# Performance work log

Hardware: AMD Instinct MI355X
Metric: run time of the kernel (lower is better)

Reference implementation:

```python
import jax, jax.numpy as jnp
import numpy as np

NUM_HEADS = 8
NUM_GROUPS = 8
EPS = 1e-5


def group_norm(x, gamma, beta):
    # x: [B, C, H, W]; normalize over (C//G, H, W) per group
    B, C, H, W = x.shape
    xg = x.reshape(B, NUM_GROUPS, C // NUM_GROUPS, H, W)
    mean = jnp.mean(xg, axis=(2, 3, 4), keepdims=True)
    var = jnp.var(xg, axis=(2, 3, 4), keepdims=True)
    xg = (xg - mean) * jax.lax.rsqrt(var + EPS)
    x = xg.reshape(B, C, H, W)
    return x * gamma[None, :, None, None] + beta[None, :, None, None]


def setup_inputs() -> dict:
    key = jax.random.key(0)
    ks = jax.random.split(key, 10)
    B, C, H, W = 16, 512, 32, 32
    s = 0.02
    return {
        "x": jax.random.normal(ks[0], (B, C, H, W), jnp.float32),
        "wq": jax.random.normal(ks[1], (C, C), jnp.float32) * s,
        "bq": jnp.zeros((C,), jnp.float32),
        "wk": jax.random.normal(ks[2], (C, C), jnp.float32) * s,
        "bk": jnp.zeros((C,), jnp.float32),
        "wv": jax.random.normal(ks[3], (C, C), jnp.float32) * s,
        "bv": jnp.zeros((C,), jnp.float32),
        "wo": jax.random.normal(ks[4], (C, C), jnp.float32) * s,
        "bo": jnp.zeros((C,), jnp.float32),
        "gamma": jnp.ones((C,), jnp.float32),
        "beta": jnp.zeros((C,), jnp.float32),
    }


def reference(x, wq, bq, wk, bk, wv, bv, wo, bo, gamma, beta):
    B, C, H, W = x.shape
    Hh = NUM_HEADS
    Dh = C // Hh
    N = H * W
    scale = Dh ** (-0.5)

    residual = x
    xn = group_norm(x, gamma, beta).reshape(B, C, N)  # [B, C, N]

    # Conv1d kernel-size-1 == channel matmul: out[b,o,n] = sum_i w[o,i] x[b,i,n] + b[o]
    q = jnp.einsum('oi,bin->bon', wq, xn) + bq[None, :, None]
    k = jnp.einsum('oi,bin->bon', wk, xn) + bk[None, :, None]
    v = jnp.einsum('oi,bin->bon', wv, xn) + bv[None, :, None]

    q = q.reshape(B, Hh, Dh, N)
    k = k.reshape(B, Hh, Dh, N)
    v = v.reshape(B, Hh, Dh, N)

    attn = jnp.einsum('bhdn,bhdm->bhnm', q, k) * scale  # [B, H, N, N]
    attn = jax.nn.softmax(attn, axis=-1)
    out = jnp.einsum('bhnm,bhdm->bhdn', attn, v)  # [B, H, Dh, N]

    out = out.reshape(B, C, N)
    out = jnp.einsum('oi,bin->bon', wo, out) + bo[None, :, None]
    return out.reshape(B, C, H, W) + residual
```

## Files before the change

### kernel.cpp

```cpp
#include <hip/hip_runtime.h>
#include <hip/hip_bf16.h>

#define BB 16
#define CC 512
#define NN 1024
#define GG 8
#define HHH 8
#define DH 64

typedef __bf16 bf16x8 __attribute__((ext_vector_type(8)));
typedef float f32x4 __attribute__((ext_vector_type(4)));
typedef float f32x16 __attribute__((ext_vector_type(16)));
typedef unsigned int u32x4 __attribute__((ext_vector_type(4)));

#define QSCALE 0.18033688011116027f

__device__ __forceinline__ unsigned short bfb(float f) {
    __hip_bfloat16 h = __float2bfloat16(f);
    return __builtin_bit_cast(unsigned short, h);
}

__device__ __forceinline__ bf16x8 ldb8(const void* p) {
    return *reinterpret_cast<const bf16x8*>(p);
}

__device__ __forceinline__ unsigned int cvtpk(float lo, float hi) {
    unsigned int r;
    asm("v_cvt_pk_bf16_f32 %0, %1, %2" : "=v"(r) : "v"(lo), "v"(hi));
    return r;
}

typedef const __attribute__((address_space(1))) unsigned int* gas_ptr;
typedef __attribute__((address_space(3))) unsigned int* las_ptr;
__device__ __forceinline__ void gload_lds16(const void* g, void* l) {
    __builtin_amdgcn_global_load_lds((gas_ptr)g, (las_ptr)l, 16, 0, 0);
}

__global__ __launch_bounds__(256) void wconv_kernel(
    const float4* __restrict__ wq, const float4* __restrict__ wk,
    const float4* __restrict__ wv, const float4* __restrict__ wo,
    ushort4* __restrict__ oq, ushort4* __restrict__ ok2,
    ushort4* __restrict__ ov, ushort4* __restrict__ oo) {
    int i = blockIdx.x * 256 + threadIdx.x;
    float4 a;
    ushort4 r;
    a = wq[i]; r.x = bfb(a.x); r.y = bfb(a.y); r.z = bfb(a.z); r.w = bfb(a.w); oq[i] = r;
    a = wk[i]; r.x = bfb(a.x); r.y = bfb(a.y); r.z = bfb(a.z); r.w = bfb(a.w); ok2[i] = r;
    a = wv[i]; r.x = bfb(a.x); r.y = bfb(a.y); r.z = bfb(a.z); r.w = bfb(a.w); ov[i] = r;
    a = wo[i]; r.x = bfb(a.x); r.y = bfb(a.y); r.z = bfb(a.z); r.w = bfb(a.w); oo[i] = r;
}

__global__ __launch_bounds__(256) void gn_kernel(
    const float* __restrict__ x, const float* __restrict__ gamma,
    const float* __restrict__ beta, unsigned short* __restrict__ xnT) {
    int b = blockIdx.x >> 3, g = blockIdx.x & 7;
    const float* xg = x + ((size_t)b * CC + g * 64) * NN;
    int t = threadIdx.x;

    float s = 0.f, s2 = 0.f;
    for (int i = 0; i < 64; ++i) {
        float4 v = reinterpret_cast<const float4*>(xg)[t + i * 256];
        s += v.x + v.y + v.z + v.w;
        s2 += v.x * v.x + v.y * v.y + v.z * v.z + v.w * v.w;
    }
    #pragma unroll
    for (int m = 1; m < 64; m <<= 1) {
        s += __shfl_xor(s, m);
        s2 += __shfl_xor(s2, m);
    }
    __shared__ float red[2][4];
    int wid = t >> 6;
    if ((t & 63) == 0) { red[0][wid] = s; red[1][wid] = s2; }
    __syncthreads();
    s = red[0][0] + red[0][1] + red[0][2] + red[0][3];
    s2 = red[1][0] + red[1][1] + red[1][2] + red[1][3];
    float mean = s * (1.f / 65536.f);
    float var = s2 * (1.f / 65536.f) - mean * mean;
    float rstd = rsqrtf(var + 1e-5f);

    __shared__ unsigned short tile[64][68];
    for (int nt = 0; nt < 16; ++nt) {
        __syncthreads();
        #pragma unroll
        for (int p = 0; p < 4; ++p) {
            int cc = p * 16 + (t >> 4);
            int nn = (t & 15) * 4;
            float4 v = *reinterpret_cast<const float4*>(&xg[(size_t)cc * NN + nt * 64 + nn]);
            float ga = gamma[g * 64 + cc], be = beta[g * 64 + cc];
            float aa = rstd * ga;
            float c0 = be - mean * aa;
            ushort4 pk;
            pk.x = bfb(v.x * aa + c0);
            pk.y = bfb(v.y * aa + c0);
            pk.z = bfb(v.z * aa + c0);
            pk.w = bfb(v.w * aa + c0);
            *reinterpret_cast<ushort4*>(&tile[cc][nn]) = pk;
        }
        __syncthreads();
        #pragma unroll
        for (int p = 0; p < 16; ++p) {
            int nn = p * 4 + (t >> 6);
            int cc = t & 63;
            xnT[((size_t)b * NN + nt * 64 + nn) * CC + g * 64 + cc] = tile[cc][nn];
        }
    }
}

__global__ __launch_bounds__(256, 2) void qkv2_kernel(
    const unsigned short* __restrict__ wqb, const unsigned short* __restrict__ wkb,
    const unsigned short* __restrict__ wvb,
    const float* __restrict__ bq, const float* __restrict__ bk, const float* __restrict__ bv,
    const unsigned short* __restrict__ xnT,
    unsigned short* __restrict__ qt, unsigned short* __restrict__ kt,
    unsigned short* __restrict__ vv) {
    int wg = blockIdx.x;
    int xcd = wg & 7, local = wg >> 3;
    int mloc = local / 12;
    int rem = local - mloc * 12;
    int n_tile = rem / 3;
    int p = rem - n_tile * 3;
    int m_tile = xcd * 16 + mloc;

    const unsigned short* w = (p == 0) ? wqb : (p == 1) ? wkb : wvb;
    const float* bias = (p == 0) ? bq : (p == 1) ? bk : bv;
    int row0 = m_tile * 128;
    int o0t = n_tile * 128;

    __shared__ __align__(16) char As[2][16384];
    __shared__ __align__(16) char Bs[2][16384];

    int t = threadIdx.x;
    int lane = t & 63, wid = t >> 6;
    int Rl = lane >> 3;
    int csw = ((lane & 7) ^ Rl) << 4;

    const char* Ag = (const char*)xnT + (size_t)row0 * 1024;
    const char* Bg = (const char*)w + (size_t)o0t * 1024;

    #pragma unroll
    for (int j = 0; j < 4; ++j) {
        int ii = wid * 4 + j;
        size_t ro = (size_t)(ii * 8 + Rl) * 1024 + csw;
        gload_lds16(Ag + ro, &As[0][ii * 1024]);
        gload_lds16(Bg + ro, &Bs[0][ii * 1024]);
    }
    __syncthreads();

    int wr = wid & 1, wc = wid >> 1;
    int lr = lane & 15, lg = lane >> 4;
    f32x4 acc[4][4] = {};

    for (int ks = 0; ks < 8; ++ks) {
        int cb_ = ks & 1;
        if (ks < 7) {
            int k0 = (ks + 1) * 64;
            #pragma unroll
            for (int j = 0; j < 4; ++j) {
                int ii = wid * 4 + j;
                size_t ro = (size_t)(ii * 8 + Rl) * 1024 + k0 * 2 + csw;
                gload_lds16(Ag + ro, &As[cb_ ^ 1][ii * 1024]);
                gload_lds16(Bg + ro, &Bs[cb_ ^ 1][ii * 1024]);
            }
        }
        const char* al = As[cb_];
        const char* bl = Bs[cb_];
        #pragma unroll
        for (int kk = 0; kk < 2; ++kk) {
            bf16x8 wf[4], xf[4];
            #pragma unroll
            for (int r = 0; r < 4; ++r) {
                int row = wc * 64 + r * 16 + lr;
                wf[r] = ldb8(bl + row * 128 + (((kk * 4 + lg) ^ (row & 7)) << 4));
            }
            #pragma unroll
            for (int c = 0; c < 4; ++c) {
                int row = wr * 64 + c * 16 + lr;
                xf[c] = ldb8(al + row * 128 + (((kk * 4 + lg) ^ (row & 7)) << 4));
            }
            __builtin_amdgcn_s_setprio(1);
            #pragma unroll
            for (int r = 0; r < 4; ++r)
                #pragma unroll
                for (int c = 0; c < 4; ++c)
                    acc[r][c] = __builtin_amdgcn_mfma_f32_16x16x32_bf16(wf[r], xf[c], acc[r][c], 0, 0, 0);
            __builtin_amdgcn_s_setprio(0);
        }
        __syncthreads();
    }

    #pragma unroll
    for (int r = 0; r < 4; ++r) {
        int o0 = o0t + wc * 64 + r * 16 + lg * 4;
        #pragma unroll
        for (int c = 0; c < 4; ++c) {
            int grow = row0 + wr * 64 + c * 16 + lr;
            int b = grow >> 10, n = grow & 1023;
            float v0 = acc[r][c][0] + bias[o0 + 0];
            float v1 = acc[r][c][1] + bias[o0 + 1];
            float v2 = acc[r][c][2] + bias[o0 + 2];
            float v3 = acc[r][c][3] + bias[o0 + 3];
            if (p < 2) {
                if (p == 0) { v0 *= QSCALE; v1 *= QSCALE; v2 *= QSCALE; v3 *= QSCALE; }
                unsigned short* outp = (p == 0) ? qt : kt;
                int h = o0 >> 6, d = o0 & 63;
                ushort4 pk;
                pk.x = bfb(v0); pk.y = bfb(v1); pk.z = bfb(v2); pk.w = bfb(v3);
                *reinterpret_cast<ushort4*>(outp + ((size_t)(b * HHH + h) * NN + n) * DH + d) = pk;
            } else {
                vv[((size_t)b * CC + o0 + 0) * NN + n] = bfb(v0);
                vv[((size_t)b * CC + o0 + 1) * NN + n] = bfb(v1);
                vv[((size_t)b * CC + o0 + 2) * NN + n] = bfb(v2);
                vv[((size_t)b * CC + o0 + 3) * NN + n] = bfb(v3);
            }
        }
    }
}

__global__ __launch_bounds__(256, 2) void attn4_kernel(
    const unsigned short* __restrict__ qt, const unsigned short* __restrict__ kt,
    const unsigned short* __restrict__ vv, unsigned short* __restrict__ aoT) {
    int wg = blockIdx.x;
    int bh = ((wg >> 6) << 3) + (wg & 7);
    int qt8 = (wg >> 3) & 7;
    int b = bh >> 3, h = bh & 7;
    int lane = threadIdx.x & 63, wid = threadIdx.x >> 6;
    int nl = lane & 31, hi = lane >> 5;
    int n = qt8 * 128 + wid * 32 + nl;

    const unsigned short* Qb = qt + (size_t)bh * NN * DH;
    const unsigned short* Kb = kt + (size_t)bh * NN * DH;
    const unsigned short* Vb = vv + ((size_t)b * CC + h * DH) * NN;

    __shared__ __align__(16) char smem[2][16384];

    const unsigned short* Qp = Qb + (size_t)n * DH + hi * 8;
    bf16x8 qf[4];
    qf[0] = ldb8(Qp);
    qf[1] = ldb8(Qp + 16);
    qf[2] = ldb8(Qp + 32);
    qf[3] = ldb8(Qp + 48);

    int Rl = lane >> 3;
    int cs16 = 16 * ((lane & 7) ^ Rl);
    const char* Kc = (const char*)Kb;
    const char* Vc = (const char*)Vb;

    #pragma unroll
    for (int j = 0; j < 2; ++j) {
        int ii = 2 * wid + j;
        int R = ii * 8 + Rl;
        gload_lds16(Kc + (size_t)R * 128 + cs16, &smem[0][ii * 1024]);
        gload_lds16(Vc + (size_t)R * 2048 + cs16, &smem[0][8192 + ii * 1024]);
    }
    __syncthreads();

    f32x16 o0 = {}, o1 = {};
    float l_i = 0.f;
    int cur = 0;

    for (int mt = 0; mt < 16; ++mt) {
        if (mt < 15) {
            int m0n = (mt + 1) * 64;
            #pragma unroll
            for (int j = 0; j < 2; ++j) {
                int ii = 2 * wid + j;
                int R = ii * 8 + Rl;
                gload_lds16(Kc + (size_t)(m0n + R) * 128 + cs16, &smem[cur ^ 1][ii * 1024]);
                gload_lds16(Vc + (size_t)R * 2048 + (size_t)m0n * 2 + cs16,
                            &smem[cur ^ 1][8192 + ii * 1024]);
            }
        }

        const char* kl = &smem[cur][0];
        const char* vl = &smem[cur][8192];
        int swz = (nl & 7) << 4;
        int rowA = nl * 128, rowB = (nl + 32) * 128;

        bf16x8 ka[4], kbf[4];
        #pragma unroll
        for (int ks = 0; ks < 4; ++ks) {
            int cb = (hi * 16 + ks * 32) ^ swz;
            ka[ks]  = ldb8(kl + rowA + cb);
            kbf[ks] = ldb8(kl + rowB + cb);
        }

        f32x16 s0 = {}, s1 = {};
        __builtin_amdgcn_s_setprio(1);
        #pragma unroll
        for (int ks = 0; ks < 4; ++ks) {
            s0 = __builtin_amdgcn_mfma_f32_32x32x16_bf16(ka[ks], qf[ks], s0, 0, 0, 0);
            s1 = __builtin_amdgcn_mfma_f32_32x32x16_bf16(kbf[ks], qf[ks], s1, 0, 0, 0);
        }
        __builtin_amdgcn_s_setprio(0);

        bf16x8 va[4], vbf[4];
        #pragma unroll
        for (int ks = 0; ks < 4; ++ks) {
            int cb = (hi * 16 + ks * 32) ^ swz;
            va[ks]  = ldb8(vl + rowA + cb);
            vbf[ks] = ldb8(vl + rowB + cb);
        }

        #pragma unroll
        for (int e = 0; e < 16; ++e) s0[e] = __builtin_amdgcn_exp2f(s0[e]);
        #pragma unroll
        for (int e = 0; e < 16; ++e) s1[e] = __builtin_amdgcn_exp2f(s1[e]);
        float ts[16];
        #pragma unroll
        for (int e = 0; e < 16; ++e) ts[e] = s0[e] + s1[e];
        #pragma unroll
        for (int st = 8; st; st >>= 1)
            #pragma unroll
            for (int e = 0; e < st; ++e) ts[e] += ts[e + st];
        l_i += ts[0];

        unsigned pA = cvtpk(s0[0], s0[1]), pB = cvtpk(s0[4], s0[5]);
        asm("v_permlane32_swap_b32 %0, %1" : "+v"(pA), "+v"(pB));
        unsigned pC = cvtpk(s0[2], s0[3]), pD = cvtpk(s0[6], s0[7]);
        asm("v_permlane32_swap_b32 %0, %1" : "+v"(pC), "+v"(pD));
        unsigned pE = cvtpk(s0[8], s0[9]), pF = cvtpk(s0[12], s0[13]);
        asm("v_permlane32_swap_b32 %0, %1" : "+v"(pE), "+v"(pF));
        unsigned pG = cvtpk(s0[10], s0[11]), pH = cvtpk(s0[14], s0[15]);
        asm("v_permlane32_swap_b32 %0, %1" : "+v"(pG), "+v"(pH));
        u32x4 w00 = {pA, pC, pB, pD};
        u32x4 w01 = {pE, pG, pF, pH};
        unsigned qA = cvtpk(s1[0], s1[1]), qB = cvtpk(s1[4], s1[5]);
        asm("v_permlane32_swap_b32 %0, %1" : "+v"(qA), "+v"(qB));
        unsigned qC = cvtpk(s1[2], s1[3]), qD = cvtpk(s1[6], s1[7]);
        asm("v_permlane32_swap_b32 %0, %1" : "+v"(qC), "+v"(qD));
        unsigned qE = cvtpk(s1[8], s1[9]), qF = cvtpk(s1[12], s1[13]);
        asm("v_permlane32_swap_b32 %0, %1" : "+v"(qE), "+v"(qF));
        unsigned qG = cvtpk(s1[10], s1[11]), qH = cvtpk(s1[14], s1[15]);
        asm("v_permlane32_swap_b32 %0, %1" : "+v"(qG), "+v"(qH));
        u32x4 w10 = {qA, qC, qB, qD};
        u32x4 w11 = {qE, qG, qF, qH};

        bf16x8 pa00 = __builtin_bit_cast(bf16x8, w00);
        bf16x8 pa01 = __builtin_bit_cast(bf16x8, w01);
        bf16x8 pa10 = __builtin_bit_cast(bf16x8, w10);
        bf16x8 pa11 = __builtin_bit_cast(bf16x8, w11);

        __builtin_amdgcn_s_setprio(1);
        o0 = __builtin_amdgcn_mfma_f32_32x32x16_bf16(va[0], pa00, o0, 0, 0, 0);
        o0 = __builtin_amdgcn_mfma_f32_32x32x16_bf16(va[1], pa01, o0, 0, 0, 0);
        o0 = __builtin_amdgcn_mfma_f32_32x32x16_bf16(va[2], pa10, o0, 0, 0, 0);
        o0 = __builtin_amdgcn_mfma_f32_32x32x16_bf16(va[3], pa11, o0, 0, 0, 0);
        o1 = __builtin_amdgcn_mfma_f32_32x32x16_bf16(vbf[0], pa00, o1, 0, 0, 0);
        o1 = __builtin_amdgcn_mfma_f32_32x32x16_bf16(vbf[1], pa01, o1, 0, 0, 0);
        o1 = __builtin_amdgcn_mfma_f32_32x32x16_bf16(vbf[2], pa10, o1, 0, 0, 0);
        o1 = __builtin_amdgcn_mfma_f32_32x32x16_bf16(vbf[3], pa11, o1, 0, 0, 0);
        __builtin_amdgcn_s_setprio(0);

        __syncthreads();
        cur ^= 1;
    }

    float l = l_i + __shfl_xor(l_i, 32);
    float inv = 1.f / l;
    unsigned short* op = aoT + ((size_t)b * NN + n) * CC + h * DH;
    #pragma unroll
    for (int q = 0; q < 4; ++q) {
        ushort4 pk;
        pk.x = bfb(o0[4 * q + 0] * inv);
        pk.y = bfb(o0[4 * q + 1] * inv);
        pk.z = bfb(o0[4 * q + 2] * inv);
        pk.w = bfb(o0[4 * q + 3] * inv);
        *reinterpret_cast<ushort4*>(op + q * 8 + hi * 4) = pk;
        ushort4 pk2;
        pk2.x = bfb(o1[4 * q + 0] * inv);
        pk2.y = bfb(o1[4 * q + 1] * inv);
        pk2.z = bfb(o1[4 * q + 2] * inv);
        pk2.w = bfb(o1[4 * q + 3] * inv);
        *reinterpret_cast<ushort4*>(op + 32 + q * 8 + hi * 4) = pk2;
    }
}

__global__ __launch_bounds__(256, 2) void oproj2_kernel(
    const unsigned short* __restrict__ wob, const float* __restrict__ bo,
    const unsigned short* __restrict__ aoT, const float* __restrict__ x,
    float* __restrict__ out) {
    int wg = blockIdx.x;
    int xcd = wg & 7, local = wg >> 3;
    int mloc = local >> 2;
    int n_tile = local & 3;
    int m_tile = xcd * 16 + mloc;
    int row0 = m_tile * 128;
    int o0t = n_tile * 128;

    __shared__ __align__(16) char As[2][16384];
    __shared__ __align__(16) char Bs[2][16384];

    int t = threadIdx.x;
    int lane = t & 63, wid = t >> 6;
    int Rl = lane >> 3;
    int csw = ((lane & 7) ^ Rl) << 4;

    const char* Ag = (const char*)aoT + (size_t)row0 * 1024;
    const char* Bg = (const char*)wob + (size_t)o0t * 1024;

    #pragma unroll
    for (int j = 0; j < 4; ++j) {
        int ii = wid * 4 + j;
        size_t ro = (size_t)(ii * 8 + Rl) * 1024 + csw;
        gload_lds16(Ag + ro, &As[0][ii * 1024]);
        gload_lds16(Bg + ro, &Bs[0][ii * 1024]);
    }
    __syncthreads();

    int wr = wid & 1, wc = wid >> 1;
    int lr = lane & 15, lg = lane >> 4;
    f32x4 acc[4][4] = {};

    for (int ks = 0; ks < 8; ++ks) {
        int cb_ = ks & 1;
        if (ks < 7) {
            int k0 = (ks + 1) * 64;
            #pragma unroll
            for (int j = 0; j < 4; ++j) {
                int ii = wid * 4 + j;
                size_t ro = (size_t)(ii * 8 + Rl) * 1024 + k0 * 2 + csw;
                gload_lds16(Ag + ro, &As[cb_ ^ 1][ii * 1024]);
                gload_lds16(Bg + ro, &Bs[cb_ ^ 1][ii * 1024]);
            }
        }
        const char* al = As[cb_];
        const char* bl = Bs[cb_];
        #pragma unroll
        for (int kk = 0; kk < 2; ++kk) {
            bf16x8 wf[4], xf[4];
            #pragma unroll
            for (int r = 0; r < 4; ++r) {
                int row = wc * 64 + r * 16 + lr;
                wf[r] = ldb8(bl + row * 128 + (((kk * 4 + lg) ^ (row & 7)) << 4));
            }
            #pragma unroll
            for (int c = 0; c < 4; ++c) {
                int row = wr * 64 + c * 16 + lr;
                xf[c] = ldb8(al + row * 128 + (((kk * 4 + lg) ^ (row & 7)) << 4));
            }
            __builtin_amdgcn_s_setprio(1);
            #pragma unroll
            for (int r = 0; r < 4; ++r)
                #pragma unroll
                for (int c = 0; c < 4; ++c)
                    acc[r][c] = __builtin_amdgcn_mfma_f32_16x16x32_bf16(wf[r], xf[c], acc[r][c], 0, 0, 0);
            __builtin_amdgcn_s_setprio(0);
        }
        __syncthreads();
    }

    #pragma unroll
    for (int r = 0; r < 4; ++r) {
        int o0 = o0t + wc * 64 + r * 16 + lg * 4;
        #pragma unroll
        for (int c = 0; c < 4; ++c) {
            int grow = row0 + wr * 64 + c * 16 + lr;
            int b = grow >> 10, n = grow & 1023;
            #pragma unroll
            for (int j = 0; j < 4; ++j) {
                size_t idx = ((size_t)b * CC + o0 + j) * NN + n;
                out[idx] = acc[r][c][j] + bo[o0 + j] + x[idx];
            }
        }
    }
}

extern "C" void kernel_launch(void* const* d_in, const int* in_sizes, int n_in,
                              void* d_out, int out_size, void* d_ws, size_t ws_size,
                              hipStream_t stream) {
    const float* x     = (const float*)d_in[0];
    const float* wq    = (const float*)d_in[1];
    const float* bq    = (const float*)d_in[2];
    const float* wk    = (const float*)d_in[3];
    const float* bk    = (const float*)d_in[4];
    const float* wv    = (const float*)d_in[5];
    const float* bv    = (const float*)d_in[6];
    const float* wo    = (const float*)d_in[7];
    const float* bo    = (const float*)d_in[8];
    const float* gamma = (const float*)d_in[9];
    const float* beta  = (const float*)d_in[10];

    char* ws = (char*)d_ws;
    const size_t WSZ = (size_t)CC * CC * 2;
    const size_t TEN = (size_t)BB * NN * CC * 2;
    unsigned short* wqb = (unsigned short*)(ws);
    unsigned short* wkb = (unsigned short*)(ws + WSZ);
    unsigned short* wvb = (unsigned short*)(ws + 2 * WSZ);
    unsigned short* wob = (unsigned short*)(ws + 3 * WSZ);
    unsigned short* xnT = (unsigned short*)(ws + 4 * WSZ);
    unsigned short* qt  = (unsigned short*)(ws + 4 * WSZ + TEN);
    unsigned short* kt  = (unsigned short*)(ws + 4 * WSZ + 2 * TEN);
    unsigned short* vv  = (unsigned short*)(ws + 4 * WSZ + 3 * TEN);
    unsigned short* aoT = (unsigned short*)(ws + 4 * WSZ + 4 * TEN);

    wconv_kernel<<<dim3(256), dim3(256), 0, stream>>>(
        (const float4*)wq, (const float4*)wk, (const float4*)wv, (const float4*)wo,
        (ushort4*)wqb, (ushort4*)wkb, (ushort4*)wvb, (ushort4*)wob);
    gn_kernel<<<dim3(128), dim3(256), 0, stream>>>(x, gamma, beta, xnT);
    qkv2_kernel<<<dim3(1536), dim3(256), 0, stream>>>(
        wqb, wkb, wvb, bq, bk, bv, xnT, qt, kt, vv);
    attn4_kernel<<<dim3(1024), dim3(256), 0, stream>>>(qt, kt, vv, aoT);
    oproj2_kernel<<<dim3(512), dim3(256), 0, stream>>>(wob, bo, aoT, x, (float*)d_out);
}
```

Before: 128.9 us.

## Split GroupNorm into parallel stats/apply passes and shrink GEMM K-tile

```diff
diff --git a/kernel.cpp b/kernel.cpp
--- a/kernel.cpp
+++ b/kernel.cpp
@@ -36,50 +36,75 @@
     __builtin_amdgcn_global_load_lds((gas_ptr)g, (las_ptr)l, 16, 0, 0);
 }
 
-__global__ __launch_bounds__(256) void wconv_kernel(
+__global__ __launch_bounds__(256) void statsconv_kernel(
+    const float* __restrict__ x,
     const float4* __restrict__ wq, const float4* __restrict__ wk,
     const float4* __restrict__ wv, const float4* __restrict__ wo,
     ushort4* __restrict__ oq, ushort4* __restrict__ ok2,
-    ushort4* __restrict__ ov, ushort4* __restrict__ oo) {
-    int i = blockIdx.x * 256 + threadIdx.x;
-    float4 a;
-    ushort4 r;
-    a = wq[i]; r.x = bfb(a.x); r.y = bfb(a.y); r.z = bfb(a.z); r.w = bfb(a.w); oq[i] = r;
-    a = wk[i]; r.x = bfb(a.x); r.y = bfb(a.y); r.z = bfb(a.z); r.w = bfb(a.w); ok2[i] = r;
-    a = wv[i]; r.x = bfb(a.x); r.y = bfb(a.y); r.z = bfb(a.z); r.w = bfb(a.w); ov[i] = r;
-    a = wo[i]; r.x = bfb(a.x); r.y = bfb(a.y); r.z = bfb(a.z); r.w = bfb(a.w); oo[i] = r;
-}
-
-__global__ __launch_bounds__(256) void gn_kernel(
+    ushort4* __restrict__ ov, ushort4* __restrict__ oo,
+    float* __restrict__ part) {
+    int blk = blockIdx.x;
+    int t = threadIdx.x;
+    if (blk < 512) {
+        int bg = blk >> 2, q = blk & 3;
+        const float* xg = x + (size_t)bg * 65536 + q * 256;
+        float s = 0.f, s2 = 0.f;
+        #pragma unroll
+        for (int i = 0; i < 16; ++i) {
+            int c = i * 256 + t;
+            int row = c >> 6, col = c & 63;
+            float4 v = *reinterpret_cast<const float4*>(xg + (size_t)row * 1024 + col * 4);
+            s += v.x + v.y + v.z + v.w;
+            s2 += v.x * v.x + v.y * v.y + v.z * v.z + v.w * v.w;
+        }
+        #pragma unroll
+        for (int m = 1; m < 64; m <<= 1) {
+            s += __shfl_xor(s, m);
+            s2 += __shfl_xor(s2, m);
+        }
+        __shared__ float red[2][4];
+        int wid = t >> 6;
+        if ((t & 63) == 0) { red[0][wid] = s; red[1][wid] = s2; }
+        __syncthreads();
+        if (t == 0) {
+            part[blk * 2 + 0] = red[0][0] + red[0][1] + red[0][2] + red[0][3];
+            part[blk * 2 + 1] = red[1][0] + red[1][1] + red[1][2] + red[1][3];
+        }
+    } else {
+        int i = (blk - 512) * 256 + t;
+        float4 a;
+        ushort4 r;
+        a = wq[i]; r.x = bfb(a.x); r.y = bfb(a.y); r.z = bfb(a.z); r.w = bfb(a.w); oq[i] = r;
+        a = wk[i]; r.x = bfb(a.x); r.y = bfb(a.y); r.z = bfb(a.z); r.w = bfb(a.w); ok2[i] = r;
+        a = wv[i]; r.x = bfb(a.x); r.y = bfb(a.y); r.z = bfb(a.z); r.w = bfb(a.w); ov[i] = r;
+        a = wo[i]; r.x = bfb(a.x); r.y = bfb(a.y); r.z = bfb(a.z); r.w = bfb(a.w); oo[i] = r;
+    }
+}
+
+__global__ __launch_bounds__(256) void gn_apply_kernel(
     const float* __restrict__ x, const float* __restrict__ gamma,
-    const float* __restrict__ beta, unsigned short* __restrict__ xnT) {
-    int b = blockIdx.x >> 3, g = blockIdx.x & 7;
-    const float* xg = x + ((size_t)b * CC + g * 64) * NN;
+    const float* __restrict__ beta, const float* __restrict__ part,
+    unsigned short* __restrict__ xnT) {
+    int blk = blockIdx.x;
+    int bg = blk >> 2, q = blk & 3;
+    int b = bg >> 3, g = bg & 7;
+    const float* xg = x + (size_t)bg * 65536;
     int t = threadIdx.x;
 
     float s = 0.f, s2 = 0.f;
-    for (int i = 0; i < 64; ++i) {
-        float4 v = reinterpret_cast<const float4*>(xg)[t + i * 256];
-        s += v.x + v.y + v.z + v.w;
-        s2 += v.x * v.x + v.y * v.y + v.z * v.z + v.w * v.w;
-    }
-    #pragma unroll
-    for (int m = 1; m < 64; m <<= 1) {
-        s += __shfl_xor(s, m);
-        s2 += __shfl_xor(s2, m);
-    }
-    __shared__ float red[2][4];
-    int wid = t >> 6;
-    if ((t & 63) == 0) { red[0][wid] = s; red[1][wid] = s2; }
-    __syncthreads();
-    s = red[0][0] + red[0][1] + red[0][2] + red[0][3];
-    s2 = red[1][0] + red[1][1] + red[1][2] + red[1][3];
+    #pragma unroll
+    for (int j = 0; j < 4; ++j) {
+        s += part[(bg * 4 + j) * 2 + 0];
+        s2 += part[(bg * 4 + j) * 2 + 1];
+    }
     float mean = s * (1.f / 65536.f);
     float var = s2 * (1.f / 65536.f) - mean * mean;
     float rstd = rsqrtf(var + 1e-5f);
 
     __shared__ unsigned short tile[64][68];
-    for (int nt = 0; nt < 16; ++nt) {
+    #pragma unroll
+    for (int i = 0; i < 4; ++i) {
+        int nt = q * 4 + i;
         __syncthreads();
         #pragma unroll
         for (int p = 0; p < 4; ++p) {
@@ -106,7 +131,7 @@
     }
 }
 
-__global__ __launch_bounds__(256, 2) void qkv2_kernel(
+__global__ __launch_bounds__(256, 2) void qkv3_kernel(
     const unsigned short* __restrict__ wqb, const unsigned short* __restrict__ wkb,
     const unsigned short* __restrict__ wvb,
     const float* __restrict__ bq, const float* __restrict__ bk, const float* __restrict__ bv,
@@ -126,23 +151,23 @@
     int row0 = m_tile * 128;
     int o0t = n_tile * 128;
 
-    __shared__ __align__(16) char As[2][16384];
-    __shared__ __align__(16) char Bs[2][16384];
+    __shared__ __align__(16) char As[2][8192];
+    __shared__ __align__(16) char Bs[2][8192];
 
     int t = threadIdx.x;
     int lane = t & 63, wid = t >> 6;
-    int Rl = lane >> 3;
-    int csw = ((lane & 7) ^ Rl) << 4;
 
     const char* Ag = (const char*)xnT + (size_t)row0 * 1024;
     const char* Bg = (const char*)w + (size_t)o0t * 1024;
 
-    #pragma unroll
-    for (int j = 0; j < 4; ++j) {
-        int ii = wid * 4 + j;
-        size_t ro = (size_t)(ii * 8 + Rl) * 1024 + csw;
-        gload_lds16(Ag + ro, &As[0][ii * 1024]);
-        gload_lds16(Bg + ro, &Bs[0][ii * 1024]);
+    int c0 = wid * 128 + lane;
+    #define SRCOFF(cj) ((size_t)((cj) >> 2) * 1024 + ((((cj) & 3) ^ (((cj) >> 3) & 3)) << 4))
+
+    #pragma unroll
+    for (int j = 0; j < 2; ++j) {
+        int cj = c0 + j * 64;
+        gload_lds16(Ag + SRCOFF(cj), &As[0][(wid * 2 + j) * 1024]);
+        gload_lds16(Bg + SRCOFF(cj), &Bs[0][(wid * 2 + j) * 1024]);
     }
     __syncthreads();
 
@@ -150,43 +175,40 @@
     int lr = lane & 15, lg = lane >> 4;
     f32x4 acc[4][4] = {};
 
-    for (int ks = 0; ks < 8; ++ks) {
+    for (int ks = 0; ks < 16; ++ks) {
         int cb_ = ks & 1;
-        if (ks < 7) {
-            int k0 = (ks + 1) * 64;
-            #pragma unroll
-            for (int j = 0; j < 4; ++j) {
-                int ii = wid * 4 + j;
-                size_t ro = (size_t)(ii * 8 + Rl) * 1024 + k0 * 2 + csw;
-                gload_lds16(Ag + ro, &As[cb_ ^ 1][ii * 1024]);
-                gload_lds16(Bg + ro, &Bs[cb_ ^ 1][ii * 1024]);
+        if (ks < 15) {
+            int k0b = (ks + 1) * 64;
+            #pragma unroll
+            for (int j = 0; j < 2; ++j) {
+                int cj = c0 + j * 64;
+                gload_lds16(Ag + SRCOFF(cj) + k0b, &As[cb_ ^ 1][(wid * 2 + j) * 1024]);
+                gload_lds16(Bg + SRCOFF(cj) + k0b, &Bs[cb_ ^ 1][(wid * 2 + j) * 1024]);
             }
         }
         const char* al = As[cb_];
         const char* bl = Bs[cb_];
-        #pragma unroll
-        for (int kk = 0; kk < 2; ++kk) {
-            bf16x8 wf[4], xf[4];
-            #pragma unroll
-            for (int r = 0; r < 4; ++r) {
-                int row = wc * 64 + r * 16 + lr;
-                wf[r] = ldb8(bl + row * 128 + (((kk * 4 + lg) ^ (row & 7)) << 4));
-            }
-            #pragma unroll
-            for (int c = 0; c < 4; ++c) {
-                int row = wr * 64 + c * 16 + lr;
-                xf[c] = ldb8(al + row * 128 + (((kk * 4 + lg) ^ (row & 7)) << 4));
-            }
-            __builtin_amdgcn_s_setprio(1);
-            #pragma unroll
-            for (int r = 0; r < 4; ++r)
-                #pragma unroll
-                for (int c = 0; c < 4; ++c)
-                    acc[r][c] = __builtin_amdgcn_mfma_f32_16x16x32_bf16(wf[r], xf[c], acc[r][c], 0, 0, 0);
-            __builtin_amdgcn_s_setprio(0);
-        }
+        bf16x8 wf[4], xf[4];
+        #pragma unroll
+        for (int r = 0; r < 4; ++r) {
+            int row = wc * 64 + r * 16 + lr;
+            wf[r] = ldb8(bl + row * 64 + (((lg ^ ((row >> 1) & 3))) << 4));
+        }
+        #pragma unroll
+        for (int c = 0; c < 4; ++c) {
+            int row = wr * 64 + c * 16 + lr;
+            xf[c] = ldb8(al + row * 64 + (((lg ^ ((row >> 1) & 3))) << 4));
+        }
+        __builtin_amdgcn_s_setprio(1);
+        #pragma unroll
+        for (int r = 0; r < 4; ++r)
+            #pragma unroll
+            for (int c = 0; c < 4; ++c)
+                acc[r][c] = __builtin_amdgcn_mfma_f32_16x16x32_bf16(wf[r], xf[c], acc[r][c], 0, 0, 0);
+        __builtin_amdgcn_s_setprio(0);
         __syncthreads();
     }
+    #undef SRCOFF
 
     #pragma unroll
     for (int r = 0; r < 4; ++r) {
@@ -375,7 +397,7 @@
     }
 }
 
-__global__ __launch_bounds__(256, 2) void oproj2_kernel(
+__global__ __launch_bounds__(256, 2) void oproj3_kernel(
     const unsigned short* __restrict__ wob, const float* __restrict__ bo,
     const unsigned short* __restrict__ aoT, const float* __restrict__ x,
     float* __restrict__ out) {
@@ -387,23 +409,23 @@
     int row0 = m_tile * 128;
     int o0t = n_tile * 128;
 
-    __shared__ __align__(16) char As[2][16384];
-    __shared__ __align__(16) char Bs[2][16384];
+    __shared__ __align__(16) char As[2][8192];
+    __shared__ __align__(16) char Bs[2][8192];
 
     int t = threadIdx.x;
     int lane = t & 63, wid = t >> 6;
-    int Rl = lane >> 3;
-    int csw = ((lane & 7) ^ Rl) << 4;
 
     const char* Ag = (const char*)aoT + (size_t)row0 * 1024;
     const char* Bg = (const char*)wob + (size_t)o0t * 1024;
 
-    #pragma unroll
-    for (int j = 0; j < 4; ++j) {
-        int ii = wid * 4 + j;
-        size_t ro = (size_t)(ii * 8 + Rl) * 1024 + csw;
-        gload_lds16(Ag + ro, &As[0][ii * 1024]);
-        gload_lds16(Bg + ro, &Bs[0][ii * 1024]);
+    int c0 = wid * 128 + lane;
+    #define SRCOFF(cj) ((size_t)((cj) >> 2) * 1024 + ((((cj) & 3) ^ (((cj) >> 3) & 3)) << 4))
+
+    #pragma unroll
+    for (int j = 0; j < 2; ++j) {
+        int cj = c0 + j * 64;
+        gload_lds16(Ag + SRCOFF(cj), &As[0][(wid * 2 + j) * 1024]);
+        gload_lds16(Bg + SRCOFF(cj), &Bs[0][(wid * 2 + j) * 1024]);
     }
     __syncthreads();
 
@@ -411,43 +433,40 @@
     int lr = lane & 15, lg = lane >> 4;
     f32x4 acc[4][4] = {};
 
-    for (int ks = 0; ks < 8; ++ks) {
+    for (int ks = 0; ks < 16; ++ks) {
         int cb_ = ks & 1;
-        if (ks < 7) {
-            int k0 = (ks + 1) * 64;
-            #pragma unroll
-            for (int j = 0; j < 4; ++j) {
-                int ii = wid * 4 + j;
-                size_t ro = (size_t)(ii * 8 + Rl) * 1024 + k0 * 2 + csw;
-                gload_lds16(Ag + ro, &As[cb_ ^ 1][ii * 1024]);
-                gload_lds16(Bg + ro, &Bs[cb_ ^ 1][ii * 1024]);
+        if (ks < 15) {
+            int k0b = (ks + 1) * 64;
+            #pragma unroll
+            for (int j = 0; j < 2; ++j) {
+                int cj = c0 + j * 64;
+                gload_lds16(Ag + SRCOFF(cj) + k0b, &As[cb_ ^ 1][(wid * 2 + j) * 1024]);
+                gload_lds16(Bg + SRCOFF(cj) + k0b, &Bs[cb_ ^ 1][(wid * 2 + j) * 1024]);
             }
         }
         const char* al = As[cb_];
         const char* bl = Bs[cb_];
-        #pragma unroll
-        for (int kk = 0; kk < 2; ++kk) {
-            bf16x8 wf[4], xf[4];
-            #pragma unroll
-            for (int r = 0; r < 4; ++r) {
-                int row = wc * 64 + r * 16 + lr;
-                wf[r] = ldb8(bl + row * 128 + (((kk * 4 + lg) ^ (row & 7)) << 4));
-            }
-            #pragma unroll
-            for (int c = 0; c < 4; ++c) {
-                int row = wr * 64 + c * 16 + lr;
-                xf[c] = ldb8(al + row * 128 + (((kk * 4 + lg) ^ (row & 7)) << 4));
-            }
-            __builtin_amdgcn_s_setprio(1);
-            #pragma unroll
-            for (int r = 0; r < 4; ++r)
-                #pragma unroll
-                for (int c = 0; c < 4; ++c)
-                    acc[r][c] = __builtin_amdgcn_mfma_f32_16x16x32_bf16(wf[r], xf[c], acc[r][c], 0, 0, 0);
-            __builtin_amdgcn_s_setprio(0);
-        }
+        bf16x8 wf[4], xf[4];
+        #pragma unroll
+        for (int r = 0; r < 4; ++r) {
+            int row = wc * 64 + r * 16 + lr;
+            wf[r] = ldb8(bl + row * 64 + (((lg ^ ((row >> 1) & 3))) << 4));
+        }
+        #pragma unroll
+        for (int c = 0; c < 4; ++c) {
+            int row = wr * 64 + c * 16 + lr;
+            xf[c] = ldb8(al + row * 64 + (((lg ^ ((row >> 1) & 3))) << 4));
+        }
+        __builtin_amdgcn_s_setprio(1);
+        #pragma unroll
+        for (int r = 0; r < 4; ++r)
+            #pragma unroll
+            for (int c = 0; c < 4; ++c)
+                acc[r][c] = __builtin_amdgcn_mfma_f32_16x16x32_bf16(wf[r], xf[c], acc[r][c], 0, 0, 0);
+        __builtin_amdgcn_s_setprio(0);
         __syncthreads();
     }
+    #undef SRCOFF
 
     #pragma unroll
     for (int r = 0; r < 4; ++r) {
@@ -492,13 +511,14 @@
     unsigned short* kt  = (unsigned short*)(ws + 4 * WSZ + 2 * TEN);
     unsigned short* vv  = (unsigned short*)(ws + 4 * WSZ + 3 * TEN);
     unsigned short* aoT = (unsigned short*)(ws + 4 * WSZ + 4 * TEN);
-
-    wconv_kernel<<<dim3(256), dim3(256), 0, stream>>>(
-        (const float4*)wq, (const float4*)wk, (const float4*)wv, (const float4*)wo,
-        (ushort4*)wqb, (ushort4*)wkb, (ushort4*)wvb, (ushort4*)wob);
-    gn_kernel<<<dim3(128), dim3(256), 0, stream>>>(x, gamma, beta, xnT);
-    qkv2_kernel<<<dim3(1536), dim3(256), 0, stream>>>(
+    float* part         = (float*)(ws + 4 * WSZ + 5 * TEN);
+
+    statsconv_kernel<<<dim3(768), dim3(256), 0, stream>>>(
+        x, (const float4*)wq, (const float4*)wk, (const float4*)wv, (const float4*)wo,
+        (ushort4*)wqb, (ushort4*)wkb, (ushort4*)wvb, (ushort4*)wob, part);
+    gn_apply_kernel<<<dim3(512), dim3(256), 0, stream>>>(x, gamma, beta, part, xnT);
+    qkv3_kernel<<<dim3(1536), dim3(256), 0, stream>>>(
         wqb, wkb, wvb, bq, bk, bv, xnT, qt, kt, vv);
     attn4_kernel<<<dim3(1024), dim3(256), 0, stream>>>(qt, kt, vv, aoT);
-    oproj2_kernel<<<dim3(512), dim3(256), 0, stream>>>(wob, bo, aoT, x, (float*)d_out);
-}
+    oproj3_kernel<<<dim3(512), dim3(256), 0, stream>>>(wob, bo, aoT, x, (float*)d_out);
+}
```

After: 127.7 us. About the same (-0.9%).

## Split group-norm stats into partial-sum blocks fused with weight conversion

Applied to the files above, without the earlier changes.

```diff
diff --git a/kernel.cpp b/kernel.cpp
--- a/kernel.cpp
+++ b/kernel.cpp
@@ -36,50 +36,75 @@
     __builtin_amdgcn_global_load_lds((gas_ptr)g, (las_ptr)l, 16, 0, 0);
 }
 
-__global__ __launch_bounds__(256) void wconv_kernel(
+__global__ __launch_bounds__(256) void statsconv_kernel(
+    const float* __restrict__ x,
     const float4* __restrict__ wq, const float4* __restrict__ wk,
     const float4* __restrict__ wv, const float4* __restrict__ wo,
     ushort4* __restrict__ oq, ushort4* __restrict__ ok2,
-    ushort4* __restrict__ ov, ushort4* __restrict__ oo) {
-    int i = blockIdx.x * 256 + threadIdx.x;
-    float4 a;
-    ushort4 r;
-    a = wq[i]; r.x = bfb(a.x); r.y = bfb(a.y); r.z = bfb(a.z); r.w = bfb(a.w); oq[i] = r;
-    a = wk[i]; r.x = bfb(a.x); r.y = bfb(a.y); r.z = bfb(a.z); r.w = bfb(a.w); ok2[i] = r;
-    a = wv[i]; r.x = bfb(a.x); r.y = bfb(a.y); r.z = bfb(a.z); r.w = bfb(a.w); ov[i] = r;
-    a = wo[i]; r.x = bfb(a.x); r.y = bfb(a.y); r.z = bfb(a.z); r.w = bfb(a.w); oo[i] = r;
-}
-
-__global__ __launch_bounds__(256) void gn_kernel(
+    ushort4* __restrict__ ov, ushort4* __restrict__ oo,
+    float* __restrict__ part) {
+    int blk = blockIdx.x;
+    int t = threadIdx.x;
+    if (blk < 512) {
+        int bg = blk >> 2, q = blk & 3;
+        const float* xg = x + (size_t)bg * 65536 + q * 256;
+        float s = 0.f, s2 = 0.f;
+        #pragma unroll
+        for (int i = 0; i < 16; ++i) {
+            int c = i * 256 + t;
+            int row = c >> 6, col = c & 63;
+            float4 v = *reinterpret_cast<const float4*>(xg + (size_t)row * 1024 + col * 4);
+            s += v.x + v.y + v.z + v.w;
+            s2 += v.x * v.x + v.y * v.y + v.z * v.z + v.w * v.w;
+        }
+        #pragma unroll
+        for (int m = 1; m < 64; m <<= 1) {
+            s += __shfl_xor(s, m);
+            s2 += __shfl_xor(s2, m);
+        }
+        __shared__ float red[2][4];
+        int wid = t >> 6;
+        if ((t & 63) == 0) { red[0][wid] = s; red[1][wid] = s2; }
+        __syncthreads();
+        if (t == 0) {
+            part[blk * 2 + 0] = red[0][0] + red[0][1] + red[0][2] + red[0][3];
+            part[blk * 2 + 1] = red[1][0] + red[1][1] + red[1][2] + red[1][3];
+        }
+    } else {
+        int i = (blk - 512) * 256 + t;
+        float4 a;
+        ushort4 r;
+        a = wq[i]; r.x = bfb(a.x); r.y = bfb(a.y); r.z = bfb(a.z); r.w = bfb(a.w); oq[i] = r;
+        a = wk[i]; r.x = bfb(a.x); r.y = bfb(a.y); r.z = bfb(a.z); r.w = bfb(a.w); ok2[i] = r;
+        a = wv[i]; r.x = bfb(a.x); r.y = bfb(a.y); r.z = bfb(a.z); r.w = bfb(a.w); ov[i] = r;
+        a = wo[i]; r.x = bfb(a.x); r.y = bfb(a.y); r.z = bfb(a.z); r.w = bfb(a.w); oo[i] = r;
+    }
+}
+
+__global__ __launch_bounds__(256) void gn_apply_kernel(
     const float* __restrict__ x, const float* __restrict__ gamma,
-    const float* __restrict__ beta, unsigned short* __restrict__ xnT) {
-    int b = blockIdx.x >> 3, g = blockIdx.x & 7;
-    const float* xg = x + ((size_t)b * CC + g * 64) * NN;
+    const float* __restrict__ beta, const float* __restrict__ part,
+    unsigned short* __restrict__ xnT) {
+    int blk = blockIdx.x;
+    int bg = blk >> 2, q = blk & 3;
+    int b = bg >> 3, g = bg & 7;
+    const float* xg = x + (size_t)bg * 65536;
     int t = threadIdx.x;
 
     float s = 0.f, s2 = 0.f;
-    for (int i = 0; i < 64; ++i) {
-        float4 v = reinterpret_cast<const float4*>(xg)[t + i * 256];
-        s += v.x + v.y + v.z + v.w;
-        s2 += v.x * v.x + v.y * v.y + v.z * v.z + v.w * v.w;
-    }
-    #pragma unroll
-    for (int m = 1; m < 64; m <<= 1) {
-        s += __shfl_xor(s, m);
-        s2 += __shfl_xor(s2, m);
-    }
-    __shared__ float red[2][4];
-    int wid = t >> 6;
-    if ((t & 63) == 0) { red[0][wid] = s; red[1][wid] = s2; }
-    __syncthreads();
-    s = red[0][0] + red[0][1] + red[0][2] + red[0][3];
-    s2 = red[1][0] + red[1][1] + red[1][2] + red[1][3];
+    #pragma unroll
+    for (int j = 0; j < 4; ++j) {
+        s += part[(bg * 4 + j) * 2 + 0];
+        s2 += part[(bg * 4 + j) * 2 + 1];
+    }
     float mean = s * (1.f / 65536.f);
     float var = s2 * (1.f / 65536.f) - mean * mean;
     float rstd = rsqrtf(var + 1e-5f);
 
     __shared__ unsigned short tile[64][68];
-    for (int nt = 0; nt < 16; ++nt) {
+    #pragma unroll
+    for (int i = 0; i < 4; ++i) {
+        int nt = q * 4 + i;
         __syncthreads();
         #pragma unroll
         for (int p = 0; p < 4; ++p) {
@@ -492,11 +517,12 @@
     unsigned short* kt  = (unsigned short*)(ws + 4 * WSZ + 2 * TEN);
     unsigned short* vv  = (unsigned short*)(ws + 4 * WSZ + 3 * TEN);
     unsigned short* aoT = (unsigned short*)(ws + 4 * WSZ + 4 * TEN);
-
-    wconv_kernel<<<dim3(256), dim3(256), 0, stream>>>(
-        (const float4*)wq, (const float4*)wk, (const float4*)wv, (const float4*)wo,
-        (ushort4*)wqb, (ushort4*)wkb, (ushort4*)wvb, (ushort4*)wob);
-    gn_kernel<<<dim3(128), dim3(256), 0, stream>>>(x, gamma, beta, xnT);
+    float* part         = (float*)(ws + 4 * WSZ + 5 * TEN);
+
+    statsconv_kernel<<<dim3(768), dim3(256), 0, stream>>>(
+        x, (const float4*)wq, (const float4*)wk, (const float4*)wv, (const float4*)wo,
+        (ushort4*)wqb, (ushort4*)wkb, (ushort4*)wvb, (ushort4*)wob, part);
+    gn_apply_kernel<<<dim3(512), dim3(256), 0, stream>>>(x, gamma, beta, part, xnT);
     qkv2_kernel<<<dim3(1536), dim3(256), 0, stream>>>(
         wqb, wkb, wvb, bq, bk, bv, xnT, qt, kt, vv);
     attn4_kernel<<<dim3(1024), dim3(256), 0, stream>>>(qt, kt, vv, aoT);
```

Result: faster. 123.3 us (-4.3%).
